# Optimization experiments

Measured on AMD Instinct MI355X. Metric: run time of the kernel, lower is better.

The kernel has to match this reference:

```python
import jax, jax.numpy as jnp
import numpy as np

B, T, D, H = 4, 2048, 2048, 16
DH = D // H

def setup_inputs() -> dict:
    key = jax.random.key(0)
    ks = jax.random.split(key, 9)
    s = 1.0 / np.sqrt(D)
    return {
        "x": jax.random.normal(ks[0], (B, T, D), dtype=jnp.float32),
        "Wq": jax.random.uniform(ks[1], (D, D), jnp.float32, -s, s),
        "bq": jax.random.uniform(ks[2], (D,), jnp.float32, -s, s),
        "Wk": jax.random.uniform(ks[3], (D, D), jnp.float32, -s, s),
        "bk": jax.random.uniform(ks[4], (D,), jnp.float32, -s, s),
        "Wv": jax.random.uniform(ks[5], (D, D), jnp.float32, -s, s),
        "bv": jax.random.uniform(ks[6], (D,), jnp.float32, -s, s),
        "Wo": jax.random.uniform(ks[7], (D, D), jnp.float32, -s, s),
        "bo": jax.random.uniform(ks[8], (D,), jnp.float32, -s, s),
    }

def reference(x, Wq, bq, Wk, bk, Wv, bv, Wo, bo):
    # projections: [B,T,D] -> [B,H,T,DH]
    def split_heads(y):
        return y.reshape(B, T, H, DH).transpose(0, 2, 1, 3)
    q = split_heads(x @ Wq + bq)
    k = split_heads(x @ Wk + bk)
    v = split_heads(x @ Wv + bv)
    scale = DH ** -0.5
    scores = jnp.einsum('bhtd,bhsd->bhts', q, k) * scale  # [B,H,T,T]
    causal = jnp.tril(jnp.ones((T, T), dtype=bool))
    scores = jnp.where(causal[None, None], scores, -jnp.inf)
    weights = jax.nn.softmax(scores, axis=-1)
    out = jnp.einsum('bhts,bhsd->bhtd', weights, v)  # [B,H,T,DH]
    out = out.transpose(0, 2, 1, 3).reshape(B, T, D)
    return out @ Wo + bo
```

## Files before the change

### kernel.cpp

```cpp
#include <hip/hip_runtime.h>
#include <hip/hip_bf16.h>

#define B_  4
#define T_  2048
#define D_  2048
#define H_  16
#define DH_ 128
#define KG  2048

typedef __attribute__((ext_vector_type(4))) float f32x4;
typedef __attribute__((ext_vector_type(8))) short short8;
typedef __attribute__((ext_vector_type(4))) _Float16 half4;

__device__ __forceinline__ ushort f2bf(float f) {
    unsigned int u = __builtin_bit_cast(unsigned int, f);
    u += 0x7fffu + ((u >> 16) & 1u);
    return (ushort)(u >> 16);
}
__device__ __forceinline__ ushort f2h(float f) {
    return (ushort)(__builtin_bit_cast(unsigned int, __builtin_amdgcn_cvt_pkrtz(f, f)) & 0xffffu);
}

__device__ __forceinline__ void glds16(const void* g, void* l) {
    __builtin_amdgcn_global_load_lds(
        (const __attribute__((address_space(1))) unsigned int*)g,
        (__attribute__((address_space(3))) unsigned int*)l, 16, 0, 0);
}

__global__ void cast_f32_bf16(const float* __restrict__ x, ushort* __restrict__ xb, int n) {
    int i = (blockIdx.x * 256 + threadIdx.x) * 4;
    if (i < n) {
        float4 v = *(const float4*)(x + i);
        ushort4 o;
        o.x = f2bf(v.x); o.y = f2bf(v.y); o.z = f2bf(v.z); o.w = f2bf(v.w);
        *(ushort4*)(xb + i) = o;
    }
}

__global__ void transpose_cast(const float* __restrict__ W, ushort* __restrict__ Wt) {
    __shared__ float tile[32][33];
    int tx = threadIdx.x, ty = threadIdx.y;
    int n0 = blockIdx.x * 32, k0 = blockIdx.y * 32;
#pragma unroll
    for (int i = 0; i < 4; i++)
        tile[ty + i * 8][tx] = W[(size_t)(k0 + ty + i * 8) * D_ + n0 + tx];
    __syncthreads();
#pragma unroll
    for (int i = 0; i < 4; i++)
        Wt[(size_t)(n0 + ty + i * 8) * D_ + k0 + tx] = f2bf(tile[tx][ty + i * 8]);
}


#define LDS_A(d, qm, AF)                                                                   \
  { const char* base_ = smem + (((d)*2 + (qm)) << 14);                                     \
    _Pragma("unroll") for (int mt = 0; mt < 4; ++mt)                                       \
      _Pragma("unroll") for (int kk = 0; kk < 2; ++kk) {                                   \
        int idx_ = wm*64 + mt*16 + l15;                                                    \
        AF[mt][kk] = __builtin_bit_cast(short8,                                            \
            *(const uint4*)(base_ + idx_*128 + (((kk*4 + quad) ^ (l15 & 7)) << 4)));       \
      } }

#define LDS_B(d, qn, BF)                                                                   \
  { const char* base_ = smem + 65536 + (((d)*2 + (qn)) << 14);                             \
    _Pragma("unroll") for (int nt = 0; nt < 2; ++nt)                                       \
      _Pragma("unroll") for (int kk = 0; kk < 2; ++kk) {                                   \
        int idx_ = wn*32 + nt*16 + l15;                                                    \
        BF[nt][kk] = __builtin_bit_cast(short8,                                            \
            *(const uint4*)(base_ + idx_*128 + (((kk*4 + quad) ^ (l15 & 7)) << 4)));       \
      } }

#define STAGE_A(d, qm, kt)                                                                 \
  { char* ld_ = smem + (((d)*2 + (qm)) << 14) + tid*16;                                    \
    const ushort* s_ = Ap + (size_t)(arow + (qm)*64) * KG + (kt)*64 + chl*8;               \
    glds16(s_, ld_);                                                                       \
    glds16(s_ + (size_t)128*KG, ld_ + 8192); }

#define STAGE_B(d, qn, kt)                                                                 \
  { char* ld_ = smem + 65536 + (((d)*2 + (qn)) << 14) + tid*16;                            \
    const ushort* s_ = Bp + (size_t)(bcol + (qn)*32) * KG + (kt)*64 + chl*8;               \
    glds16(s_, ld_);                                                                       \
    glds16(s_ + (size_t)128*KG, ld_ + 8192); }

#define MFMA16(QM, QN, AF, BF)                                                             \
  __builtin_amdgcn_s_setprio(1);                                                           \
  _Pragma("unroll") for (int mt = 0; mt < 4; ++mt)                                         \
    _Pragma("unroll") for (int nt = 0; nt < 2; ++nt)                                       \
      _Pragma("unroll") for (int kk = 0; kk < 2; ++kk)                                     \
        acc[(QM)*4 + mt][(QN)*2 + nt] = __builtin_amdgcn_mfma_f32_16x16x32_bf16(           \
            AF[mt][kk], BF[nt][kk], acc[(QM)*4 + mt][(QN)*2 + nt], 0, 0, 0);               \
  __builtin_amdgcn_s_setprio(0);

#define BAR1_LGKM  __builtin_amdgcn_s_barrier();                                           \
                   asm volatile("s_waitcnt lgkmcnt(0)" ::: "memory");
#define BAR2       __builtin_amdgcn_s_barrier();
#define VM4        asm volatile("s_waitcnt vmcnt(4)" ::: "memory");
#define VM0        asm volatile("s_waitcnt vmcnt(0)" ::: "memory");

#define GEMM256_MAIN_LOOP                                                                  \
    f32x4 acc[8][4] = {};                                                                  \
    short8 aF[4][2], bF0[2][2], bF1[2][2];                                                 \
                               \
    STAGE_B(0, 0, 0); STAGE_A(0, 0, 0); STAGE_A(0, 1, 0); STAGE_B(0, 1, 0);                \
    STAGE_B(1, 0, 1); STAGE_A(1, 0, 1);                                                    \
    VM4; __builtin_amdgcn_s_barrier();                                                     \
    _Pragma("unroll 1")                                                                    \
    for (int j = 0; j < 16; ++j) {                                                         \
        const int t1 = 2*j + 1;                                                            \
        const int t2 = (2*j + 2 < 32) ? 2*j + 2 : 31;                                      \
        const int t3 = (2*j + 3 < 32) ? 2*j + 3 : 31;                                      \
         LDS_A(0, 0, aF); LDS_B(0, 0, bF0); STAGE_A(1, 1, t1);                     \
                 BAR1_LGKM; MFMA16(0, 0, aF, bF0); BAR2;                                   \
         LDS_B(0, 1, bF1); STAGE_B(1, 1, t1);                                      \
                 BAR1_LGKM; MFMA16(0, 1, aF, bF1); BAR2;                                   \
         LDS_A(0, 1, aF); STAGE_B(0, 0, t2);                                       \
                 BAR1_LGKM; MFMA16(1, 1, aF, bF1); BAR2;                                   \
         STAGE_A(0, 0, t2);                                                        \
                 BAR1_LGKM; MFMA16(1, 0, aF, bF0); VM4; BAR2;                              \
         LDS_A(1, 0, aF); LDS_B(1, 0, bF0); STAGE_A(0, 1, t2);                     \
                 BAR1_LGKM; MFMA16(0, 0, aF, bF0); BAR2;                                   \
         LDS_B(1, 1, bF1); STAGE_B(0, 1, t2);                                      \
                 BAR1_LGKM; MFMA16(0, 1, aF, bF1); BAR2;                                   \
         LDS_A(1, 1, aF); STAGE_B(1, 0, t3);                                       \
                 BAR1_LGKM; MFMA16(1, 1, aF, bF1); BAR2;                                   \
         STAGE_A(1, 0, t3);                                                        \
                 BAR1_LGKM; MFMA16(1, 0, aF, bF0); VM4; BAR2;                              \
    }                                                                                      \
    VM0; __builtin_amdgcn_s_barrier();

__global__ __launch_bounds__(512, 2) void gemm_qkv256(
    const ushort* __restrict__ A,
    const ushort* __restrict__ Wq, const ushort* __restrict__ Wk, const ushort* __restrict__ Wv,
    const float* __restrict__ bq, const float* __restrict__ bk, const float* __restrict__ bv,
    ushort* __restrict__ Qb, ushort* __restrict__ Kb, ushort* __restrict__ Vtb,
    float qscale)
{
    extern __shared__ char smem[];
    const int tid = threadIdx.x;

    int id = blockIdx.y * 24 + blockIdx.x;
    id = (id & 7) * 96 + (id >> 3);
    const int bx = id % 24, by = id / 24;

    const int sel  = bx >> 3;
    const int row0 = by * 256, col0 = (bx & 7) * 256;
    const ushort* Ap = A;
    const ushort* Bp = (sel == 0) ? Wq : (sel == 1) ? Wk : Wv;
    const float* bias = (sel == 0) ? bq : (sel == 1) ? bk : bv;
    const float oscale = (sel == 0) ? qscale : 1.0f;

    const int lane = tid & 63, w = tid >> 6;
    const int l15 = lane & 15, quad = lane >> 4;
    const int wm = w & 1, wn = w >> 1;

    const int irow = tid >> 3;
    const int chl  = (tid & 7) ^ (irow & 7);
    const int arow = row0 + irow;
    const int bcol = col0 + ((irow >> 5) << 6) + (irow & 31);

    GEMM256_MAIN_LOOP

    if (sel < 2) {
        ushort* Cout = sel ? Kb : Qb;
#pragma unroll
        for (int ntg = 0; ntg < 4; ++ntg) {
            int col = col0 + wn * 64 + ntg * 16 + l15;
            float bb = bias[col];
#pragma unroll
            for (int mtg = 0; mtg < 8; ++mtg) {
                int rowb = row0 + wm * 128 + mtg * 16 + quad * 4;
#pragma unroll
                for (int r = 0; r < 4; ++r)
                    Cout[(size_t)(rowb + r) * D_ + col] = f2bf((acc[mtg][ntg][r] + bb) * oscale);
            }
        }
    } else {
        const int b = row0 >> 11, t0 = (row0 & (T_ - 1)) + wm * 128;
        const int h = (col0 + wn * 64) >> 7;
        ushort* eT = (ushort*)smem + w * (32 * 136);
#pragma unroll 1
        for (int rnd = 0; rnd < 2; ++rnd) {
#pragma unroll
            for (int ni = 0; ni < 2; ++ni) {
                int ntg = rnd * 2 + ni;
                int col = col0 + wn * 64 + ntg * 16 + l15;
                float bb = bias[col];
#pragma unroll
                for (int mtg = 0; mtg < 8; ++mtg)
#pragma unroll
                    for (int r = 0; r < 4; ++r)
                        eT[(ni * 16 + l15) * 136 + mtg * 16 + quad * 4 + r] = f2h(acc[mtg][ntg][r] + bb);
            }
            int dhbase = ((wn & 1) ? 64 : 0) + rnd * 32;
#pragma unroll
            for (int it = 0; it < 8; ++it) {
                int chunk = it * 64 + lane;
                int d2 = chunk >> 4, c = chunk & 15;
                uint4 v = *(const uint4*)(eT + d2 * 136 + c * 8);
                *(uint4*)(Vtb + (size_t)((b * H_ + h) * DH_ + dhbase + d2) * T_ + t0 + c * 8) = v;
            }
        }
    }
}

__global__ __launch_bounds__(512, 2) void gemm_o256(
    const ushort* __restrict__ A, const ushort* __restrict__ Bt,
    const float* __restrict__ bias, float* __restrict__ Cout)
{
    extern __shared__ char smem[];
    const int tid = threadIdx.x;

    int id = blockIdx.y * 8 + blockIdx.x;
    id = (id & 7) * 32 + (id >> 3);
    const int bx = id % 8, by = id / 8;

    const int row0 = by * 256, col0 = bx * 256;
    const ushort* Ap = A;
    const ushort* Bp = Bt;

    const int lane = tid & 63, w = tid >> 6;
    const int l15 = lane & 15, quad = lane >> 4;
    const int wm = w & 1, wn = w >> 1;

    const int irow = tid >> 3;
    const int chl  = (tid & 7) ^ (irow & 7);
    const int arow = row0 + irow;
    const int bcol = col0 + ((irow >> 5) << 6) + (irow & 31);

    GEMM256_MAIN_LOOP

#pragma unroll
    for (int ntg = 0; ntg < 4; ++ntg) {
        int col = col0 + wn * 64 + ntg * 16 + l15;
        float bb = bias[col];
#pragma unroll
        for (int mtg = 0; mtg < 8; ++mtg) {
            int rowb = row0 + wm * 128 + mtg * 16 + quad * 4;
#pragma unroll
            for (int r = 0; r < 4; ++r)
                Cout[(size_t)(rowb + r) * D_ + col] = acc[mtg][ntg][r] + bb;
        }
    }
}

__global__ __launch_bounds__(256, 5) void attn_kernel(
    const ushort* __restrict__ Q, const ushort* __restrict__ K,
    const ushort* __restrict__ Vt, ushort* __restrict__ O)
{
    __shared__ __align__(16) char smem[32768];
    uint4*  kS = (uint4*)smem;
    ushort* vS = (ushort*)(smem + 16384);

    const int tid = threadIdx.x;
    const int bid = blockIdx.x;
    const int slot = bid >> 3;
    const int g = (bid & 7) + 8 * (slot >> 4);
    const int qx = slot & 15;
    const int b = g >> 4, h = g & 15;

    const int lane = tid & 63, w = tid >> 6, l15 = lane & 15, quad = lane >> 4;

    const int krow = tid >> 4;
    const int kchunk = (tid & 15) ^ (krow & 7);
    const ushort* kg = K + ((size_t)(b * T_) + krow) * D_ + h * DH_ + kchunk * 8;

    const int vrow = tid >> 3, vc = tid & 7;
    const ushort* vg = Vt + ((size_t)((b * H_ + h) * DH_) + vrow) * T_ + vc * 8;
    const int vs0 = ((2 * vc    ) ^ (vrow & 15)) * 4;
    const int vs1 = ((2 * vc + 1) ^ (vrow & 15)) * 4;

    const int qts[2] = { qx, 31 - qx };

    for (int e = 0; e < 2; ++e) {
        const int qt = qts[e], q0 = qt * 64;
        const int qbase = q0 + w * 16;

        short8 aq[4];
        {
            const ushort* qp = Q + ((size_t)(b * T_) + qbase + l15) * D_ + h * DH_ + quad * 8;
#pragma unroll
            for (int ks = 0; ks < 4; ++ks)
                aq[ks] = __builtin_bit_cast(short8, *(const uint4*)(qp + ks * 32));
        }

        f32x4 accO[8] = {};
        float mrow = -INFINITY, lrow = 0.f;

        auto tile = [&](int s0, int stMax, bool diag) {
            __syncthreads();
            const ushort* kp = kg + (size_t)s0 * D_;
#pragma unroll
            for (int j = 0; j < 4; ++j) glds16(kp + (size_t)j * 16 * D_, kS + j * 256 + tid);
            const ushort* vp = vg + s0;
            uint4 vv[4];
#pragma unroll
            for (int j = 0; j < 4; ++j) vv[j] = *(const uint4*)(vp + (size_t)j * 32 * T_);
#pragma unroll
            for (int j = 0; j < 4; ++j) {
                ushort* dst = vS + (j * 32 + vrow) * 64;
                *(uint2*)(dst + vs0) = make_uint2(vv[j].x, vv[j].y);
                *(uint2*)(dst + vs1) = make_uint2(vv[j].z, vv[j].w);
            }
            __syncthreads();

            f32x4 sT[4] = {};
#pragma unroll
            for (int ks = 0; ks < 4; ++ks)
#pragma unroll
                for (int st = 0; st < 4; ++st)
                    if (st < stMax) {
                        int row = st * 16 + l15;
                        short8 ak = __builtin_bit_cast(short8, kS[row * 16 + ((ks * 4 + quad) ^ (row & 7))]);
                        sT[st] = __builtin_amdgcn_mfma_f32_16x16x32_bf16(ak, aq[ks], sT[st], 0, 0, 0);
                    }

            if (diag) {
                const int q = qbase + l15;
                const int st = stMax - 1;
#pragma unroll
                for (int r = 0; r < 4; ++r)
                    if (s0 + st * 16 + quad * 4 + r > q) sT[st][r] = -INFINITY;
            }

            float rmax = -INFINITY;
#pragma unroll
            for (int st = 0; st < 4; ++st)
                if (st < stMax)
#pragma unroll
                    for (int r = 0; r < 4; ++r) rmax = fmaxf(rmax, sT[st][r]);
            rmax = fmaxf(rmax, __shfl_xor(rmax, 16));
            rmax = fmaxf(rmax, __shfl_xor(rmax, 32));
            float mnew  = fmaxf(mrow, rmax);
            float alpha = __builtin_amdgcn_exp2f(mrow - mnew);
            mrow = mnew;

            float psum = 0.f;
            half4 pb[4];
#pragma unroll
            for (int st = 0; st < 4; ++st)
                if (st < stMax) {
                    float p0 = __builtin_amdgcn_exp2f(sT[st][0] - mnew);
                    float p1 = __builtin_amdgcn_exp2f(sT[st][1] - mnew);
                    float p2 = __builtin_amdgcn_exp2f(sT[st][2] - mnew);
                    float p3 = __builtin_amdgcn_exp2f(sT[st][3] - mnew);
                    psum += (p0 + p1) + (p2 + p3);
                    uint2 u;
                    u.x = __builtin_bit_cast(unsigned int, __builtin_amdgcn_cvt_pkrtz(p0, p1));
                    u.y = __builtin_bit_cast(unsigned int, __builtin_amdgcn_cvt_pkrtz(p2, p3));
                    pb[st] = __builtin_bit_cast(half4, u);
                }
            psum += __shfl_xor(psum, 16);
            psum += __shfl_xor(psum, 32);
            lrow = lrow * alpha + psum;
#pragma unroll
            for (int nt = 0; nt < 8; ++nt)
#pragma unroll
                for (int r = 0; r < 4; ++r) accO[nt][r] *= alpha;

#pragma unroll
            for (int st = 0; st < 4; ++st)
                if (st < stMax) {
#pragma unroll
                    for (int nt = 0; nt < 8; ++nt) {
                        int dh = nt * 16 + l15;
                        half4 vf = *(const half4*)(vS + dh * 64 + (((st * 4 + quad) ^ l15) * 4));
                        accO[nt] = __builtin_amdgcn_mfma_f32_16x16x16f16(vf, pb[st], accO[nt], 0, 0, 0);
                    }
                }
        };

        for (int it = 0; it < qt; ++it) tile(it * 64, 4, false);
        tile(qt * 64, w + 1, true);

        __syncthreads();
        ushort* eT = (ushort*)smem + w * 2176;
        float inv = 1.0f / lrow;
#pragma unroll
        for (int nt = 0; nt < 8; ++nt) {
            int dh = nt * 16 + quad * 4;
#pragma unroll
            for (int r = 0; r < 4; ++r)
                eT[l15 * 136 + dh + r] = f2bf(accO[nt][r] * inv);
        }
        for (int idx = lane; idx < 256; idx += 64) {
            int row = idx >> 4, c = idx & 15;
            uint4 v = *(const uint4*)(eT + row * 136 + c * 8);
            *(uint4*)(O + ((size_t)(b * T_) + q0 + w * 16 + row) * D_ + h * DH_ + c * 8) = v;
        }
    }
}

extern "C" void kernel_launch(void* const* d_in, const int* in_sizes, int n_in,
                              void* d_out, int out_size, void* d_ws, size_t ws_size,
                              hipStream_t stream) {
    const float* x  = (const float*)d_in[0];
    const float* Wq = (const float*)d_in[1];
    const float* bq = (const float*)d_in[2];
    const float* Wk = (const float*)d_in[3];
    const float* bk = (const float*)d_in[4];
    const float* Wv = (const float*)d_in[5];
    const float* bv = (const float*)d_in[6];
    const float* Wo = (const float*)d_in[7];
    const float* bo = (const float*)d_in[8];

    char* ws = (char*)d_ws;
    const size_t MB = 1u << 20;
    ushort* xb  = (ushort*)(ws);
    ushort* Wqt = (ushort*)(ws + 32 * MB);
    ushort* Wkt = (ushort*)(ws + 40 * MB);
    ushort* Wvt = (ushort*)(ws + 48 * MB);
    ushort* Wot = (ushort*)(ws + 56 * MB);
    ushort* Qb  = (ushort*)(ws + 64 * MB);
    ushort* Kb  = (ushort*)(ws + 96 * MB);
    ushort* Vtb = (ushort*)(ws + 128 * MB);
    ushort* Ob  = (ushort*)(ws + 160 * MB);

    const int M = B_ * T_;
    const float qscale = (float)(0.08838834764831845 * 1.4426950408889634);

    static bool attr_done = false;
    if (!attr_done) {
        (void)hipFuncSetAttribute((const void*)gemm_qkv256,
                                  hipFuncAttributeMaxDynamicSharedMemorySize, 131072);
        (void)hipFuncSetAttribute((const void*)gemm_o256,
                                  hipFuncAttributeMaxDynamicSharedMemorySize, 131072);
        attr_done = true;
    }

    cast_f32_bf16<<<(M * D_) / 1024, 256, 0, stream>>>(x, xb, M * D_);
    dim3 tb(32, 8), tg(D_ / 32, D_ / 32);
    transpose_cast<<<tg, tb, 0, stream>>>(Wq, Wqt);
    transpose_cast<<<tg, tb, 0, stream>>>(Wk, Wkt);
    transpose_cast<<<tg, tb, 0, stream>>>(Wv, Wvt);
    transpose_cast<<<tg, tb, 0, stream>>>(Wo, Wot);

    gemm_qkv256<<<dim3(24, M / 256), 512, 131072, stream>>>(
        xb, Wqt, Wkt, Wvt, bq, bk, bv, Qb, Kb, Vtb, qscale);

    attn_kernel<<<dim3(1024), 256, 0, stream>>>(Qb, Kb, Vtb, Ob);

    gemm_o256<<<dim3(D_ / 256, M / 256), 512, 131072, stream>>>(
        Ob, Wot, bo, (float*)d_out);
}
```

Measured before the change: 680.4 us.

## Precompute LDS/global addresses and reorder GEMM staging with single B fragment buffer

```diff
diff --git a/kernel.cpp b/kernel.cpp
--- a/kernel.cpp
+++ b/kernel.cpp
@@ -52,34 +52,32 @@
 
 
 #define LDS_A(d, qm, AF)                                                                   \
-  { const char* base_ = smem + (((d)*2 + (qm)) << 14);                                     \
-    _Pragma("unroll") for (int mt = 0; mt < 4; ++mt)                                       \
-      _Pragma("unroll") for (int kk = 0; kk < 2; ++kk) {                                   \
-        int idx_ = wm*64 + mt*16 + l15;                                                    \
-        AF[mt][kk] = __builtin_bit_cast(short8,                                            \
-            *(const uint4*)(base_ + idx_*128 + (((kk*4 + quad) ^ (l15 & 7)) << 4)));       \
-      } }
+  { _Pragma("unroll") for (int mt = 0; mt < 4; ++mt) {                                     \
+      AF[mt][0] = __builtin_bit_cast(short8,                                               \
+          *(const uint4*)(smem + aAddr0 + (((d)*2 + (qm)) << 14) + mt*2048));              \
+      AF[mt][1] = __builtin_bit_cast(short8,                                               \
+          *(const uint4*)(smem + aAddr1 + (((d)*2 + (qm)) << 14) + mt*2048));              \
+    } }
 
 #define LDS_B(d, qn, BF)                                                                   \
-  { const char* base_ = smem + 65536 + (((d)*2 + (qn)) << 14);                             \
-    _Pragma("unroll") for (int nt = 0; nt < 2; ++nt)                                       \
-      _Pragma("unroll") for (int kk = 0; kk < 2; ++kk) {                                   \
-        int idx_ = wn*32 + nt*16 + l15;                                                    \
-        BF[nt][kk] = __builtin_bit_cast(short8,                                            \
-            *(const uint4*)(base_ + idx_*128 + (((kk*4 + quad) ^ (l15 & 7)) << 4)));       \
-      } }
+  { _Pragma("unroll") for (int nt = 0; nt < 2; ++nt) {                                     \
+      BF[nt][0] = __builtin_bit_cast(short8,                                               \
+          *(const uint4*)(smem + bAddr0 + (((d)*2 + (qn)) << 14) + nt*2048));              \
+      BF[nt][1] = __builtin_bit_cast(short8,                                               \
+          *(const uint4*)(smem + bAddr1 + (((d)*2 + (qn)) << 14) + nt*2048));              \
+    } }
 
 #define STAGE_A(d, qm, kt)                                                                 \
-  { char* ld_ = smem + (((d)*2 + (qm)) << 14) + tid*16;                                    \
-    const ushort* s_ = Ap + (size_t)(arow + (qm)*64) * KG + (kt)*64 + chl*8;               \
-    glds16(s_, ld_);                                                                       \
-    glds16(s_ + (size_t)128*KG, ld_ + 8192); }
+  { const ushort* s_ = aSrc + (size_t)(qm) * (64 * KG) + (size_t)(kt) * 64;                \
+    char* l_ = ldsT + (((d)*2 + (qm)) << 14);                                              \
+    glds16(s_, l_);                                                                        \
+    glds16(s_ + (size_t)128 * KG, l_ + 8192); }
 
 #define STAGE_B(d, qn, kt)                                                                 \
-  { char* ld_ = smem + 65536 + (((d)*2 + (qn)) << 14) + tid*16;                            \
-    const ushort* s_ = Bp + (size_t)(bcol + (qn)*32) * KG + (kt)*64 + chl*8;               \
-    glds16(s_, ld_);                                                                       \
-    glds16(s_ + (size_t)128*KG, ld_ + 8192); }
+  { const ushort* s_ = bSrc + (size_t)(qn) * (32 * KG) + (size_t)(kt) * 64;                \
+    char* l_ = ldsT + 65536 + (((d)*2 + (qn)) << 14);                                      \
+    glds16(s_, l_);                                                                        \
+    glds16(s_ + (size_t)128 * KG, l_ + 8192); }
 
 #define MFMA16(QM, QN, AF, BF)                                                             \
   __builtin_amdgcn_s_setprio(1);                                                           \
@@ -94,36 +92,53 @@
                    asm volatile("s_waitcnt lgkmcnt(0)" ::: "memory");
 #define BAR2       __builtin_amdgcn_s_barrier();
 #define VM4        asm volatile("s_waitcnt vmcnt(4)" ::: "memory");
+#define VM2        asm volatile("s_waitcnt vmcnt(2)" ::: "memory");
 #define VM0        asm volatile("s_waitcnt vmcnt(0)" ::: "memory");
+
+#define GEMM256_PRE                                                                        \
+    const int lane = tid & 63, w = tid >> 6;                                               \
+    const int l15 = lane & 15, quad = lane >> 4;                                           \
+    const int wm = w & 1, wn = w >> 1;                                                     \
+    const int irow = tid >> 3;                                                             \
+    const int chl  = (tid & 7) ^ (irow & 7);                                               \
+    const ushort* aSrc = Ap + (size_t)(row0 + irow) * KG + chl * 8;                        \
+    const ushort* bSrc = Bp + (size_t)(col0 + ((irow >> 5) << 6) + (irow & 31)) * KG + chl * 8; \
+    char* ldsT = smem + tid * 16;                                                          \
+    const int sw0 = (quad ^ (l15 & 7)) << 4;                                               \
+    const int sw1 = ((4 + quad) ^ (l15 & 7)) << 4;                                         \
+    const int aRow = (wm * 64 + l15) * 128;                                                \
+    const int bRow = (wn * 32 + l15) * 128;                                                \
+    const int aAddr0 = aRow + sw0, aAddr1 = aRow + sw1;                                    \
+    const int bAddr0 = 65536 + bRow + sw0, bAddr1 = 65536 + bRow + sw1;
 
 #define GEMM256_MAIN_LOOP                                                                  \
     f32x4 acc[8][4] = {};                                                                  \
-    short8 aF[4][2], bF0[2][2], bF1[2][2];                                                 \
-                               \
-    STAGE_B(0, 0, 0); STAGE_A(0, 0, 0); STAGE_A(0, 1, 0); STAGE_B(0, 1, 0);                \
-    STAGE_B(1, 0, 1); STAGE_A(1, 0, 1);                                                    \
-    VM4; __builtin_amdgcn_s_barrier();                                                     \
+    short8 aF[4][2], bF[2][2];                                                             \
+    STAGE_A(0, 0, 0); STAGE_B(0, 0, 0); STAGE_A(0, 1, 0); STAGE_B(0, 1, 0);                \
+    STAGE_A(1, 0, 1);                                                                      \
+    VM2; __builtin_amdgcn_s_barrier();                                                     \
     _Pragma("unroll 1")                                                                    \
     for (int j = 0; j < 16; ++j) {                                                         \
         const int t1 = 2*j + 1;                                                            \
         const int t2 = (2*j + 2 < 32) ? 2*j + 2 : 31;                                      \
         const int t3 = (2*j + 3 < 32) ? 2*j + 3 : 31;                                      \
-         LDS_A(0, 0, aF); LDS_B(0, 0, bF0); STAGE_A(1, 1, t1);                     \
-                 BAR1_LGKM; MFMA16(0, 0, aF, bF0); BAR2;                                   \
-         LDS_B(0, 1, bF1); STAGE_B(1, 1, t1);                                      \
-                 BAR1_LGKM; MFMA16(0, 1, aF, bF1); BAR2;                                   \
-         LDS_A(0, 1, aF); STAGE_B(0, 0, t2);                                       \
-                 BAR1_LGKM; MFMA16(1, 1, aF, bF1); BAR2;                                   \
-         STAGE_A(0, 0, t2);                                                        \
-                 BAR1_LGKM; MFMA16(1, 0, aF, bF0); VM4; BAR2;                              \
-         LDS_A(1, 0, aF); LDS_B(1, 0, bF0); STAGE_A(0, 1, t2);                     \
-                 BAR1_LGKM; MFMA16(0, 0, aF, bF0); BAR2;                                   \
-         LDS_B(1, 1, bF1); STAGE_B(0, 1, t2);                                      \
-                 BAR1_LGKM; MFMA16(0, 1, aF, bF1); BAR2;                                   \
-         LDS_A(1, 1, aF); STAGE_B(1, 0, t3);                                       \
-                 BAR1_LGKM; MFMA16(1, 1, aF, bF1); BAR2;                                   \
-         STAGE_A(1, 0, t3);                                                        \
-                 BAR1_LGKM; MFMA16(1, 0, aF, bF0); VM4; BAR2;                              \
+         LDS_A(0, 0, aF); LDS_B(0, 0, bF);                                         \
+                 STAGE_A(1, 1, t1); STAGE_B(1, 0, t1);                                     \
+                 BAR1_LGKM; MFMA16(0, 0, aF, bF); BAR2;                                    \
+         LDS_B(0, 1, bF); STAGE_B(1, 1, t1);                                       \
+                 BAR1_LGKM; MFMA16(0, 1, aF, bF); BAR2;                                    \
+         LDS_A(0, 1, aF); STAGE_A(0, 0, t2);                                       \
+                 BAR1_LGKM; MFMA16(1, 1, aF, bF); BAR2;                                    \
+         LDS_B(0, 0, bF); STAGE_A(0, 1, t2);                                       \
+                 BAR1_LGKM; MFMA16(1, 0, aF, bF); VM4; BAR2;                               \
+         LDS_A(1, 0, aF); LDS_B(1, 0, bF); STAGE_B(0, 0, t2);                      \
+                 BAR1_LGKM; MFMA16(0, 0, aF, bF); BAR2;                                    \
+         LDS_B(1, 1, bF); STAGE_B(0, 1, t2);                                       \
+                 BAR1_LGKM; MFMA16(0, 1, aF, bF); BAR2;                                    \
+         LDS_A(1, 1, aF); STAGE_A(1, 0, t3);                                       \
+                 BAR1_LGKM; MFMA16(1, 1, aF, bF); BAR2;                                    \
+         LDS_B(1, 0, bF);                                                          \
+                 BAR1_LGKM; MFMA16(1, 0, aF, bF); VM2; BAR2;                               \
     }                                                                                      \
     VM0; __builtin_amdgcn_s_barrier();
 
@@ -148,15 +163,7 @@
     const float* bias = (sel == 0) ? bq : (sel == 1) ? bk : bv;
     const float oscale = (sel == 0) ? qscale : 1.0f;
 
-    const int lane = tid & 63, w = tid >> 6;
-    const int l15 = lane & 15, quad = lane >> 4;
-    const int wm = w & 1, wn = w >> 1;
-
-    const int irow = tid >> 3;
-    const int chl  = (tid & 7) ^ (irow & 7);
-    const int arow = row0 + irow;
-    const int bcol = col0 + ((irow >> 5) << 6) + (irow & 31);
-
+    GEMM256_PRE
     GEMM256_MAIN_LOOP
 
     if (sel < 2) {
@@ -217,15 +224,7 @@
     const ushort* Ap = A;
     const ushort* Bp = Bt;
 
-    const int lane = tid & 63, w = tid >> 6;
-    const int l15 = lane & 15, quad = lane >> 4;
-    const int wm = w & 1, wn = w >> 1;
-
-    const int irow = tid >> 3;
-    const int chl  = (tid & 7) ^ (irow & 7);
-    const int arow = row0 + irow;
-    const int bcol = col0 + ((irow >> 5) << 6) + (irow & 31);
-
+    GEMM256_PRE
     GEMM256_MAIN_LOOP
 
 #pragma unroll
```

Result: no change. 683.6 us (+0.5%).
